# Kernel tuning notes

Measured on AMD Instinct MI355X. Metric: run time of the kernel, lower is better.

## Reference

```python
import jax, jax.numpy as jnp
import numpy as np
import math

EMBED_DIM = 512
NUM_HEADS = 8
B, T = 1, 4096

def setup_inputs() -> dict:
    key = jax.random.key(0)
    ks = jax.random.split(key, 12)
    D = EMBED_DIM
    s = 1.0 / math.sqrt(D)
    inp = {
        "x": jax.random.normal(ks[0], (B, T, D), dtype=jnp.float32),
        "ln1_scale": jnp.ones((D,), jnp.float32),
        "ln1_bias": jnp.zeros((D,), jnp.float32),
        "Wq": jax.random.normal(ks[1], (D, D), jnp.float32) * s,
        "bq": jnp.zeros((D,), jnp.float32),
        "Wk": jax.random.normal(ks[2], (D, D), jnp.float32) * s,
        "bk": jnp.zeros((D,), jnp.float32),
        "Wv": jax.random.normal(ks[3], (D, D), jnp.float32) * s,
        "bv": jnp.zeros((D,), jnp.float32),
        "Wo": jax.random.normal(ks[4], (D, D), jnp.float32) * s,
        "bo": jnp.zeros((D,), jnp.float32),
        "ln2_scale": jnp.ones((D,), jnp.float32),
        "ln2_bias": jnp.zeros((D,), jnp.float32),
        "W1": jax.random.normal(ks[5], (D, 4 * D), jnp.float32) * s,
        "b1": jnp.zeros((4 * D,), jnp.float32),
        "W2": jax.random.normal(ks[6], (4 * D, D), jnp.float32) * (1.0 / math.sqrt(4 * D)),
        "b2": jnp.zeros((D,), jnp.float32),
    }
    return inp

def _layernorm(x, scale, bias, eps=1e-6):
    mu = jnp.mean(x, axis=-1, keepdims=True)
    var = jnp.mean(jnp.square(x - mu), axis=-1, keepdims=True)
    return (x - mu) * jax.lax.rsqrt(var + eps) * scale + bias

def reference(x, ln1_scale, ln1_bias, Wq, bq, Wk, bk, Wv, bv, Wo, bo,
              ln2_scale, ln2_bias, W1, b1, W2, b2):
    Bb, Tt, D = x.shape
    H = NUM_HEADS
    hd = D // H
    residual = x
    h = _layernorm(x, ln1_scale, ln1_bias)
    q = (h @ Wq + bq).reshape(Bb, Tt, H, hd).transpose(0, 2, 1, 3)
    k = (h @ Wk + bk).reshape(Bb, Tt, H, hd).transpose(0, 2, 1, 3)
    v = (h @ Wv + bv).reshape(Bb, Tt, H, hd).transpose(0, 2, 1, 3)
    # [B,H,T,T] scores (naive attention as in the original module)
    scores = jnp.einsum('bhqd,bhkd->bhqk', q, k) / math.sqrt(hd)
    probs = jax.nn.softmax(scores, axis=-1)
    out = jnp.einsum('bhqk,bhkd->bhqd', probs, v).transpose(0, 2, 1, 3).reshape(Bb, Tt, D)
    h = out @ Wo + bo  # dropout deterministic -> identity
    x = h + residual
    residual = x
    h = _layernorm(x, ln2_scale, ln2_bias)
    h = jax.nn.gelu(h @ W1 + b1, approximate=True)
    h = h @ W2 + b2
    return h + residual
```

## Files before the change

kernel.cpp:

```cpp
#include <hip/hip_runtime.h>
#include <hip/hip_bf16.h>
#include <stdint.h>

typedef __bf16 bf16;
typedef __bf16 bf16x4 __attribute__((ext_vector_type(4)));
typedef __bf16 bf16x8 __attribute__((ext_vector_type(8)));
typedef float  f32x4  __attribute__((ext_vector_type(4)));
typedef float  f32x16 __attribute__((ext_vector_type(16)));

#define MFMA32(A_, B_, C_) __builtin_amdgcn_mfma_f32_32x32x16_bf16((A_), (B_), (C_), 0, 0, 0)

#define QSCALE 0.1803368801111137f

__device__ __forceinline__ void gload_lds16(const void* g, void* l) {
  __builtin_amdgcn_global_load_lds(
      (const __attribute__((address_space(1))) unsigned int*)g,
      (__attribute__((address_space(3))) unsigned int*)l, 16, 0, 0);
}

__device__ __forceinline__ unsigned pk2(float lo, float hi_) {
  union { bf16 h[2]; unsigned u; } t;
  t.h[0] = (bf16)lo; t.h[1] = (bf16)hi_;
  return t.u;
}

__device__ __forceinline__ float fast_exp2(float x) {
#if __has_builtin(__builtin_amdgcn_exp2f)
  return __builtin_amdgcn_exp2f(x);
#else
  return exp2f(x);
#endif
}

__global__ __launch_bounds__(256) void prep_ln(const float* __restrict__ Wq,
                                               const float* __restrict__ Wk,
                                               const float* __restrict__ Wv,
                                               const float* __restrict__ Wo,
                                               const float* __restrict__ W1,
                                               const float* __restrict__ W2,
                                               const float* __restrict__ bq,
                                               const float* __restrict__ bk,
                                               const float* __restrict__ bv,
                                               bf16* __restrict__ wqkvT, bf16* __restrict__ woT,
                                               bf16* __restrict__ w1T, bf16* __restrict__ w2T,
                                               float* __restrict__ bqkv,
                                               const float* __restrict__ x,
                                               const float* __restrict__ ln1s,
                                               const float* __restrict__ ln1b,
                                               bf16* __restrict__ h) {
  const int b = blockIdx.x;
  if (b >= 774) {
    const int w = threadIdx.x >> 6, l = threadIdx.x & 63;
    const int row = (b - 774) * 4 + w;
    const float4* xp = (const float4*)(x + (size_t)row * 512 + l * 8);
    float4 v0 = xp[0], v1 = xp[1];
    float xv[8] = {v0.x, v0.y, v0.z, v0.w, v1.x, v1.y, v1.z, v1.w};
    float s = 0.f, q = 0.f;
#pragma unroll
    for (int j = 0; j < 8; ++j) { s += xv[j]; q += xv[j] * xv[j]; }
#pragma unroll
    for (int m = 1; m < 64; m <<= 1) { s += __shfl_xor(s, m); q += __shfl_xor(q, m); }
    const float mean = s * (1.f / 512.f);
    const float var = q * (1.f / 512.f) - mean * mean;
    const float rstd = rsqrtf(var + 1e-6f);
    const float4* scp = (const float4*)(ln1s + l * 8);
    const float4* bip = (const float4*)(ln1b + l * 8);
    float4 s0 = scp[0], s1 = scp[1], b0 = bip[0], b1 = bip[1];
    float sv[8] = {s0.x, s0.y, s0.z, s0.w, s1.x, s1.y, s1.z, s1.w};
    float bvv[8] = {b0.x, b0.y, b0.z, b0.w, b1.x, b1.y, b1.z, b1.w};
    bf16x8 ov;
#pragma unroll
    for (int j = 0; j < 8; ++j) ov[j] = (bf16)((xv[j] - mean) * rstd * sv[j] + bvv[j]);
    *(bf16x8*)(h + (size_t)row * 512 + l * 8) = ov;
    return;
  }
  if (b >= 768) {
    int i = (b - 768) * 256 + threadIdx.x;
    if (i < 1536)
      bqkv[i] = (i < 512) ? bq[i] * QSCALE : (i < 1024 ? bk[i - 512] : bv[i - 1024]);
    return;
  }
  const float* in; bf16* outp; int K, N, t; float sc = 1.f;
  if (b < 64)       { in = Wq; outp = wqkvT;              K = 512;  N = 512;  t = b;       sc = QSCALE; }
  else if (b < 128) { in = Wk; outp = wqkvT + 512 * 512;  K = 512;  N = 512;  t = b - 64;  }
  else if (b < 192) { in = Wv; outp = wqkvT + 1024 * 512; K = 512;  N = 512;  t = b - 128; }
  else if (b < 256) { in = Wo; outp = woT;                K = 512;  N = 512;  t = b - 192; }
  else if (b < 512) { in = W1; outp = w1T;                K = 512;  N = 2048; t = b - 256; }
  else              { in = W2; outp = w2T;                K = 2048; N = 512;  t = b - 512; }
  const int tx = K >> 6;
  const int k0 = (t % tx) * 64, n0 = (t / tx) * 64;
  __shared__ bf16 tile[64][72];
  const int tid = threadIdx.x;
#pragma unroll
  for (int s = 0; s < 16; ++s) {
    int j = tid + s * 256;
    int r = j >> 6, c = j & 63;
    tile[r][c] = (bf16)(in[(size_t)(k0 + r) * N + n0 + c] * sc);
  }
  __syncthreads();
#pragma unroll
  for (int s = 0; s < 16; ++s) {
    int j = tid + s * 256;
    int n = j >> 6, k = j & 63;
    outp[(size_t)(n0 + n) * K + k0 + k] = tile[k][n];
  }
}

__global__ __launch_bounds__(256) void ln_k(const float* __restrict__ x,
                                            const float* __restrict__ sc,
                                            const float* __restrict__ bi,
                                            bf16* __restrict__ out) {
  const int w = threadIdx.x >> 6, l = threadIdx.x & 63;
  const int row = blockIdx.x * 4 + w;
  const float4* xp = (const float4*)(x + (size_t)row * 512 + l * 8);
  float4 v0 = xp[0], v1 = xp[1];
  float xv[8] = {v0.x, v0.y, v0.z, v0.w, v1.x, v1.y, v1.z, v1.w};
  float s = 0.f, q = 0.f;
#pragma unroll
  for (int j = 0; j < 8; ++j) { s += xv[j]; q += xv[j] * xv[j]; }
#pragma unroll
  for (int m = 1; m < 64; m <<= 1) { s += __shfl_xor(s, m); q += __shfl_xor(q, m); }
  const float mean = s * (1.f / 512.f);
  const float var = q * (1.f / 512.f) - mean * mean;
  const float rstd = rsqrtf(var + 1e-6f);
  const float4* scp = (const float4*)(sc + l * 8);
  const float4* bip = (const float4*)(bi + l * 8);
  float4 s0 = scp[0], s1 = scp[1], b0 = bip[0], b1 = bip[1];
  float sv[8] = {s0.x, s0.y, s0.z, s0.w, s1.x, s1.y, s1.z, s1.w};
  float bvv[8] = {b0.x, b0.y, b0.z, b0.w, b1.x, b1.y, b1.z, b1.w};
  bf16x8 ov;
#pragma unroll
  for (int j = 0; j < 8; ++j) ov[j] = (bf16)((xv[j] - mean) * rstd * sv[j] + bvv[j]);
  *(bf16x8*)(out + (size_t)row * 512 + l * 8) = ov;
}

template <int EPI>
__global__ __launch_bounds__(256, 3) void gemm32(const bf16* __restrict__ A,
                                                 const bf16* __restrict__ Bt,
                                                 const float* __restrict__ bias,
                                                 const float* __restrict__ res,
                                                 void* __restrict__ outp,
                                                 bf16* __restrict__ k2,
                                                 bf16* __restrict__ v2,
                                                 int M, int N, int K) {
  __shared__ bf16 a_lds[3][64 * 64];
  __shared__ bf16 b_lds[3][64 * 64];
  const int m0 = blockIdx.x * 64, n0 = blockIdx.y * 64;
  const int tid = threadIdx.x, l = tid & 63, w = tid >> 6;
  const int wm = w >> 1, wn = w & 1;
  const int hi = l >> 5, l5 = l & 31;
  const int lr = l >> 3;
  const int cs = (l & 7) ^ (lr & 7);
  const int swl = l5 & 7;

  const bf16* ag = A + (size_t)(m0 + w * 16 + lr) * K + cs * 8;
  const bf16* bg = Bt + (size_t)(n0 + w * 16 + lr) * K + cs * 8;
  const size_t r8 = (size_t)8 * K;

#define GS32(B_)                                                   \
  do {                                                             \
    gload_lds16(ag,      (char*)a_lds[(B_)] + (w * 16) * 128);     \
    gload_lds16(ag + r8, (char*)a_lds[(B_)] + (w * 16 + 8) * 128); \
    gload_lds16(bg,      (char*)b_lds[(B_)] + (w * 16) * 128);     \
    gload_lds16(bg + r8, (char*)b_lds[(B_)] + (w * 16 + 8) * 128); \
    ag += 64; bg += 64;                                            \
  } while (0)

  f32x16 acc = {};
  const int kiters = K >> 6;
  GS32(0);
  GS32(1);
  asm volatile("s_waitcnt vmcnt(4)" ::: "memory");
  __builtin_amdgcn_s_barrier();
  for (int kt = 0; kt < kiters; ++kt) {
    if (kt + 2 < kiters) GS32((kt + 2) % 3);
    const bf16* ab = a_lds[kt % 3] + (wm * 32 + l5) * 64;
    const bf16* bb = b_lds[kt % 3] + (wn * 32 + l5) * 64;
#pragma unroll
    for (int kk = 0; kk < 4; ++kk) {
      bf16x8 af = *(const bf16x8*)(ab + ((kk * 2 + hi) ^ swl) * 8);
      bf16x8 bf_ = *(const bf16x8*)(bb + ((kk * 2 + hi) ^ swl) * 8);
      acc = MFMA32(bf_, af, acc);
    }
    if (kt + 1 < kiters) {
      if (kt + 2 < kiters) asm volatile("s_waitcnt vmcnt(4)" ::: "memory");
      else                 asm volatile("s_waitcnt vmcnt(0)" ::: "memory");
      __builtin_amdgcn_s_barrier();
    }
  }
#undef GS32

  const int row = m0 + wm * 32 + l5;
  if constexpr (EPI == 1 || EPI == 2) {
#pragma unroll
    for (int rg = 0; rg < 4; ++rg) {
      const int cb = n0 + wn * 32 + rg * 8 + hi * 4;
      float4 bb4 = *(const float4*)(bias + cb);
      float v[4];
      v[0] = acc[rg * 4 + 0] + bb4.x;
      v[1] = acc[rg * 4 + 1] + bb4.y;
      v[2] = acc[rg * 4 + 2] + bb4.z;
      v[3] = acc[rg * 4 + 3] + bb4.w;
      if constexpr (EPI == 1) {
        float4 rr = *(const float4*)(res + (size_t)row * N + cb);
        *(float4*)((float*)outp + (size_t)row * N + cb) =
            make_float4(v[0] + rr.x, v[1] + rr.y, v[2] + rr.z, v[3] + rr.w);
      } else {
        bf16x4 o;
#pragma unroll
        for (int e = 0; e < 4; ++e) {
          float t = -2.3022077697f * (v[e] + 0.044715f * v[e] * v[e] * v[e]);
          o[e] = (bf16)(v[e] / (1.f + fast_exp2(t)));
        }
        *(bf16x4*)((bf16*)outp + (size_t)row * N + cb) = o;
      }
    }
  } else {
    __syncthreads();
    bf16(*ct)[72] = (bf16(*)[72])a_lds;
    const int rl = wm * 32 + l5;
#pragma unroll
    for (int rg = 0; rg < 4; ++rg) {
      const int cl = wn * 32 + rg * 8 + hi * 4;
      float4 bb4 = *(const float4*)(bias + n0 + cl);
      bf16x4 o;
      o[0] = (bf16)(acc[rg * 4 + 0] + bb4.x);
      o[1] = (bf16)(acc[rg * 4 + 1] + bb4.y);
      o[2] = (bf16)(acc[rg * 4 + 2] + bb4.z);
      o[3] = (bf16)(acc[rg * 4 + 3] + bb4.w);
      *(bf16x4*)(&ct[rl][cl]) = o;
    }
    __syncthreads();
    if (n0 < 512) {
#pragma unroll
      for (int p = 0; p < 2; ++p) {
        int idx = p * 256 + tid;
        int r = idx >> 3, c = (idx & 7) * 8;
        *(bf16x8*)((bf16*)outp + (size_t)(m0 + r) * 512 + n0 + c) =
            *(const bf16x8*)(&ct[r][c]);
      }
    } else if (n0 < 1024) {
      bf16* kb = k2 + (size_t)((n0 - 512) >> 6) * 262144 + (size_t)m0 * 64;
#pragma unroll
      for (int p = 0; p < 2; ++p) {
        int idx = p * 256 + tid;
        int r = idx >> 3, c = (idx & 7) * 8;
        *(bf16x8*)(kb + r * 64 + c) = *(const bf16x8*)(&ct[r][c]);
      }
    } else {
      bf16* vb = v2 + (size_t)((n0 - 1024) >> 6) * 262144 + (size_t)(m0 >> 5) * 2048;
      const int d = tid >> 2, t8 = (tid & 3) * 8;
#pragma unroll
      for (int p = 0; p < 2; ++p) {
        bf16x8 vv;
#pragma unroll
        for (int e = 0; e < 8; ++e) vv[e] = ct[p * 32 + t8 + e][d];
        *(bf16x8*)(vb + p * 2048 + d * 32 + t8) = vv;
      }
    }
  }
}

__global__ __launch_bounds__(512, 4) void attn_k(const bf16* __restrict__ q2,
                                                 const bf16* __restrict__ k2,
                                                 const bf16* __restrict__ v2,
                                                 bf16* __restrict__ attnb) {
  const int bid = blockIdx.x;
  const int head = bid & 7;
  const int qt = bid >> 3;
  const int w = threadIdx.x >> 6, l = threadIdx.x & 63;
  const int hi = l >> 5, l5 = l & 31;
  const int pair = w >> 1, wq = w & 1;

  __shared__ __align__(16) char smem[65536];
  char* kt_l = smem + pair * 16384;
  char* vt_l = kt_l + 8192;

  const int qrow0 = qt * 64 + wq * 32;
  const bf16* qb = q2 + (size_t)(qrow0 + l5) * 512 + head * 64;
  bf16x8 qf[4];
#pragma unroll
  for (int cc = 0; cc < 4; ++cc) qf[cc] = *(const bf16x8*)(qb + cc * 16 + hi * 8);

  const int kstart = pair * 1024;

  const int lr = l >> 3;
  const int lc3 = (l & 7) ^ lr;
  const char* kg = (const char*)k2 + (size_t)head * 524288 + (size_t)kstart * 128 +
                   (wq * 16 + lr) * 128 + lc3 * 16;
  const char* vg = (const char*)v2 + (size_t)head * 524288 + (size_t)(kstart >> 5) * 4096 +
                   (lc3 >> 2) * 2048 + (wq * 16 + lr) * 64 + (lc3 & 3) * 16;
  const int kdst = wq * 2048;

#define STAGE(B_)                                                            \
  do {                                                                       \
    gload_lds16(kg,        kt_l + (B_) * 4096 + kdst);                       \
    gload_lds16(kg + 1024, kt_l + (B_) * 4096 + kdst + 1024);                \
    gload_lds16(vg,        vt_l + (B_) * 4096 + kdst);                       \
    gload_lds16(vg + 512,  vt_l + (B_) * 4096 + kdst + 1024);                \
    kg += 4096; vg += 4096;                                                  \
  } while (0)

  STAGE(0);
  __syncthreads();

  f32x16 o0 = {}, o1 = {};
  float psum = 0.f;
  const int swl = l5 & 7;
  const char* kbase = kt_l + l5 * 128;
  const char* vbase = vt_l + l5 * 128;

  for (int t = 0; t < 32; ++t) {
    const int cur = t & 1;
    if (t < 31) STAGE(cur ^ 1);

    __builtin_amdgcn_s_setprio(1);
    f32x16 s = {};
#pragma unroll
    for (int cc = 0; cc < 4; ++cc) {
      bf16x8 kf = *(const bf16x8*)(kbase + cur * 4096 + ((cc * 2 + hi) ^ swl) * 16);
      s = MFMA32(kf, qf[cc], s);
    }
    __builtin_amdgcn_s_setprio(0);

#pragma unroll
    for (int c = 0; c < 2; ++c) {
      float p[8];
#pragma unroll
      for (int j = 0; j < 8; ++j) p[j] = fast_exp2(s[c * 8 + j]);
      psum += ((p[0] + p[1]) + (p[2] + p[3])) + ((p[4] + p[5]) + (p[6] + p[7]));
      unsigned X = pk2(p[0], p[1]), X2 = pk2(p[2], p[3]);
      unsigned Y = pk2(p[4], p[5]), Y2 = pk2(p[6], p[7]);
      asm volatile("v_permlane32_swap_b32 %0, %1" : "+v"(X), "+v"(Y));
      asm volatile("v_permlane32_swap_b32 %0, %1" : "+v"(X2), "+v"(Y2));
      union { unsigned wd[4]; bf16x8 v; } pa;
      pa.wd[0] = X; pa.wd[1] = X2; pa.wd[2] = Y; pa.wd[3] = Y2;
      bf16x8 vf0 = *(const bf16x8*)(vbase + cur * 4096 + ((c * 2 + hi) ^ swl) * 16);
      bf16x8 vf1 = *(const bf16x8*)(vbase + cur * 4096 + ((4 + c * 2 + hi) ^ swl) * 16);
      __builtin_amdgcn_s_setprio(1);
      o0 = MFMA32(vf0, pa.v, o0);
      o1 = MFMA32(vf1, pa.v, o1);
      __builtin_amdgcn_s_setprio(0);
    }
    __syncthreads();
  }
#undef STAGE

  float* comb = (float*)smem;
  if (pair > 0) {
    float* cb = comb + (((pair - 1) * 2 + wq) * 64 + l) * 33;
#pragma unroll
    for (int r = 0; r < 16; ++r) { cb[r] = o0[r]; cb[16 + r] = o1[r]; }
    cb[32] = psum;
  }
  __syncthreads();
  if (pair == 0) {
#pragma unroll
    for (int p = 0; p < 3; ++p) {
      const float* cb = comb + ((p * 2 + wq) * 64 + l) * 33;
#pragma unroll
      for (int r = 0; r < 16; ++r) { o0[r] += cb[r]; o1[r] += cb[16 + r]; }
      psum += cb[32];
    }
    const float lsum = psum + __shfl_xor(psum, 32);
    const float inv = 1.f / lsum;
    bf16* ob = attnb + (size_t)(qrow0 + l5) * 512 + head * 64;
#pragma unroll
    for (int dt = 0; dt < 2; ++dt)
#pragma unroll
      for (int rg = 0; rg < 4; ++rg) {
        bf16x4 vv;
#pragma unroll
        for (int e = 0; e < 4; ++e) {
          const float ov = (dt == 0) ? o0[rg * 4 + e] : o1[rg * 4 + e];
          vv[e] = (bf16)(ov * inv);
        }
        *(bf16x4*)(ob + dt * 32 + rg * 8 + hi * 4) = vv;
      }
  }
}

extern "C" void kernel_launch(void* const* d_in, const int* in_sizes, int n_in,
                              void* d_out, int out_size, void* d_ws, size_t ws_size,
                              hipStream_t stream) {
  const float* x    = (const float*)d_in[0];
  const float* ln1s = (const float*)d_in[1];
  const float* ln1b = (const float*)d_in[2];
  const float* Wq   = (const float*)d_in[3];
  const float* bq   = (const float*)d_in[4];
  const float* Wk   = (const float*)d_in[5];
  const float* bk   = (const float*)d_in[6];
  const float* Wv   = (const float*)d_in[7];
  const float* bv   = (const float*)d_in[8];
  const float* Wo   = (const float*)d_in[9];
  const float* bo   = (const float*)d_in[10];
  const float* ln2s = (const float*)d_in[11];
  const float* ln2b = (const float*)d_in[12];
  const float* W1   = (const float*)d_in[13];
  const float* b1   = (const float*)d_in[14];
  const float* W2   = (const float*)d_in[15];
  const float* b2   = (const float*)d_in[16];
  float* out = (float*)d_out;

  char* ws = (char*)d_ws;
  bf16*  wqkvT = (bf16*)(ws + 0);
  bf16*  woT   = (bf16*)(ws + 1572864);
  bf16*  w1T   = (bf16*)(ws + 2097152);
  bf16*  w2T   = (bf16*)(ws + 4194304);
  float* bqkv  = (float*)(ws + 6291456);
  float* x2    = (float*)(ws + 6297600);
  bf16*  h     = (bf16*)(ws + 14686208);
  bf16*  q2    = (bf16*)(ws + 18880512);
  bf16*  k2    = (bf16*)(ws + 23074816);
  bf16*  v2    = (bf16*)(ws + 27269120);
  bf16*  attnb = h;
  bf16*  h2    = h;
  bf16*  gbuf  = (bf16*)(ws + 18880512);

  prep_ln<<<1798, 256, 0, stream>>>(Wq, Wk, Wv, Wo, W1, W2, bq, bk, bv,
                                    wqkvT, woT, w1T, w2T, bqkv, x, ln1s, ln1b, h);
  gemm32<3><<<dim3(64, 24), 256, 0, stream>>>(h, wqkvT, bqkv, nullptr, q2, k2, v2,
                                              4096, 1536, 512);
  attn_k<<<512, 512, 0, stream>>>(q2, k2, v2, attnb);
  gemm32<1><<<dim3(64, 8), 256, 0, stream>>>(attnb, woT, bo, x, x2, nullptr, nullptr,
                                             4096, 512, 512);
  ln_k<<<1024, 256, 0, stream>>>(x2, ln2s, ln2b, h2);
  gemm32<2><<<dim3(64, 32), 256, 0, stream>>>(h2, w1T, b1, nullptr, gbuf, nullptr, nullptr,
                                              4096, 2048, 512);
  gemm32<1><<<dim3(64, 8), 256, 0, stream>>>(gbuf, w2T, b2, x2, out, nullptr, nullptr,
                                             4096, 512, 2048);
}
```

Before: 140.2 us.

## Add 128x128-tile GEMM kernel for QKV and FFN-up projections

Adds a new GEMM kernel with 128x128 output tiles, where each wave computes a 2x2 grid of 32x32 MFMA tiles, and uses it for the QKV projection and the W1+GELU GEMM. The small 64x64 kernel is kept only for the residual-epilogue GEMMs. The aim is more operand reuse per LDS load and fewer total blocks and global loads for the wider-N GEMMs. The cost is more accumulator registers and fewer blocks: the QKV launch drops to 384 blocks, which may underfill the GPU. The K and V scatter epilogues are rewritten so one tile covers two heads.

Result: faster. 133.0 us (-5.1%).

```diff
diff --git a/kernel.cpp b/kernel.cpp
--- a/kernel.cpp
+++ b/kernel.cpp
@@ -140,8 +140,6 @@
                                                  const float* __restrict__ bias,
                                                  const float* __restrict__ res,
                                                  void* __restrict__ outp,
-                                                 bf16* __restrict__ k2,
-                                                 bf16* __restrict__ v2,
                                                  int M, int N, int K) {
   __shared__ bf16 a_lds[3][64 * 64];
   __shared__ bf16 b_lds[3][64 * 64];
@@ -191,71 +189,161 @@
 #undef GS32
 
   const int row = m0 + wm * 32 + l5;
-  if constexpr (EPI == 1 || EPI == 2) {
-#pragma unroll
-    for (int rg = 0; rg < 4; ++rg) {
-      const int cb = n0 + wn * 32 + rg * 8 + hi * 4;
-      float4 bb4 = *(const float4*)(bias + cb);
-      float v[4];
-      v[0] = acc[rg * 4 + 0] + bb4.x;
-      v[1] = acc[rg * 4 + 1] + bb4.y;
-      v[2] = acc[rg * 4 + 2] + bb4.z;
-      v[3] = acc[rg * 4 + 3] + bb4.w;
-      if constexpr (EPI == 1) {
-        float4 rr = *(const float4*)(res + (size_t)row * N + cb);
-        *(float4*)((float*)outp + (size_t)row * N + cb) =
-            make_float4(v[0] + rr.x, v[1] + rr.y, v[2] + rr.z, v[3] + rr.w);
-      } else {
-        bf16x4 o;
-#pragma unroll
-        for (int e = 0; e < 4; ++e) {
-          float t = -2.3022077697f * (v[e] + 0.044715f * v[e] * v[e] * v[e]);
-          o[e] = (bf16)(v[e] / (1.f + fast_exp2(t)));
+#pragma unroll
+  for (int rg = 0; rg < 4; ++rg) {
+    const int cb = n0 + wn * 32 + rg * 8 + hi * 4;
+    float4 bb4 = *(const float4*)(bias + cb);
+    float v[4];
+    v[0] = acc[rg * 4 + 0] + bb4.x;
+    v[1] = acc[rg * 4 + 1] + bb4.y;
+    v[2] = acc[rg * 4 + 2] + bb4.z;
+    v[3] = acc[rg * 4 + 3] + bb4.w;
+    float4 rr = *(const float4*)(res + (size_t)row * N + cb);
+    *(float4*)((float*)outp + (size_t)row * N + cb) =
+        make_float4(v[0] + rr.x, v[1] + rr.y, v[2] + rr.z, v[3] + rr.w);
+  }
+}
+
+template <int EPI>
+__global__ __launch_bounds__(256, 3) void gemm_w(const bf16* __restrict__ A,
+                                                 const bf16* __restrict__ Bt,
+                                                 const float* __restrict__ bias,
+                                                 void* __restrict__ outp,
+                                                 bf16* __restrict__ k2,
+                                                 bf16* __restrict__ v2,
+                                                 int M, int N, int K) {
+  __shared__ __align__(16) char smem[49152];
+  char* a_lds = smem;
+  char* b_lds = smem + 24576;
+  const int tid = threadIdx.x, l = tid & 63, w = tid >> 6;
+  const int wm = w >> 1, wn = w & 1;
+  const int hi = l >> 5, l5 = l & 31;
+  const int m0 = blockIdx.x * 128, n0 = blockIdx.y * 128;
+  const int swl = l5 & 7;
+
+  const int sr = tid >> 3, sp = tid & 7;
+  const int slc = sp ^ (sr & 7);
+  const int shalf = slc >> 2, skc = slc & 3;
+  const bf16* ag = A + (size_t)(m0 + shalf * 64 + sr) * K + skc * 8;
+  const bf16* bg = Bt + (size_t)(n0 + shalf * 64 + sr) * K + skc * 8;
+  const size_t r32 = (size_t)32 * K;
+
+#define GSW(B_)                                                       \
+  do {                                                                \
+    gload_lds16(ag,       a_lds + (B_) * 8192 + w * 1024);            \
+    gload_lds16(ag + r32, a_lds + (B_) * 8192 + 4096 + w * 1024);     \
+    gload_lds16(bg,       b_lds + (B_) * 8192 + w * 1024);            \
+    gload_lds16(bg + r32, b_lds + (B_) * 8192 + 4096 + w * 1024);     \
+    ag += 32; bg += 32;                                               \
+  } while (0)
+
+  f32x16 acc00 = {}, acc01 = {}, acc10 = {}, acc11 = {};
+  const int kiters = K >> 5;
+  GSW(0);
+  GSW(1);
+  asm volatile("s_waitcnt vmcnt(4)" ::: "memory");
+  __builtin_amdgcn_s_barrier();
+  for (int kt = 0; kt < kiters; ++kt) {
+    if (kt + 2 < kiters) GSW((kt + 2) % 3);
+    const char* ab = a_lds + (kt % 3) * 8192;
+    const char* bb = b_lds + (kt % 3) * 8192;
+#pragma unroll
+    for (int kk = 0; kk < 2; ++kk) {
+      bf16x8 af0 = *(const bf16x8*)(ab + (l5)*128      + ((wm * 4 + kk * 2 + hi) ^ swl) * 16);
+      bf16x8 af1 = *(const bf16x8*)(ab + (32 + l5)*128 + ((wm * 4 + kk * 2 + hi) ^ swl) * 16);
+      bf16x8 bf0 = *(const bf16x8*)(bb + (l5)*128      + ((wn * 4 + kk * 2 + hi) ^ swl) * 16);
+      bf16x8 bf1 = *(const bf16x8*)(bb + (32 + l5)*128 + ((wn * 4 + kk * 2 + hi) ^ swl) * 16);
+      acc00 = MFMA32(bf0, af0, acc00);
+      acc01 = MFMA32(bf1, af0, acc01);
+      acc10 = MFMA32(bf0, af1, acc10);
+      acc11 = MFMA32(bf1, af1, acc11);
+    }
+    if (kt + 1 < kiters) {
+      if (kt + 2 < kiters) asm volatile("s_waitcnt vmcnt(4)" ::: "memory");
+      else                 asm volatile("s_waitcnt vmcnt(0)" ::: "memory");
+      __builtin_amdgcn_s_barrier();
+    }
+  }
+#undef GSW
+
+  if constexpr (EPI == 2) {
+#pragma unroll
+    for (int mi = 0; mi < 2; ++mi) {
+      const int row = m0 + wm * 64 + mi * 32 + l5;
+#pragma unroll
+      for (int ni = 0; ni < 2; ++ni) {
+        const f32x16& ac = (mi == 0) ? (ni == 0 ? acc00 : acc01)
+                                     : (ni == 0 ? acc10 : acc11);
+#pragma unroll
+        for (int rg = 0; rg < 4; ++rg) {
+          const int cb = n0 + wn * 64 + ni * 32 + rg * 8 + hi * 4;
+          float4 bb4 = *(const float4*)(bias + cb);
+          float v[4] = {ac[rg * 4 + 0] + bb4.x, ac[rg * 4 + 1] + bb4.y,
+                        ac[rg * 4 + 2] + bb4.z, ac[rg * 4 + 3] + bb4.w};
+          bf16x4 o;
+#pragma unroll
+          for (int e = 0; e < 4; ++e) {
+            float t = -2.3022077697f * (v[e] + 0.044715f * v[e] * v[e] * v[e]);
+            o[e] = (bf16)(v[e] / (1.f + fast_exp2(t)));
+          }
+          *(bf16x4*)((bf16*)outp + (size_t)row * N + cb) = o;
         }
-        *(bf16x4*)((bf16*)outp + (size_t)row * N + cb) = o;
       }
     }
   } else {
     __syncthreads();
-    bf16(*ct)[72] = (bf16(*)[72])a_lds;
-    const int rl = wm * 32 + l5;
-#pragma unroll
-    for (int rg = 0; rg < 4; ++rg) {
-      const int cl = wn * 32 + rg * 8 + hi * 4;
-      float4 bb4 = *(const float4*)(bias + n0 + cl);
-      bf16x4 o;
-      o[0] = (bf16)(acc[rg * 4 + 0] + bb4.x);
-      o[1] = (bf16)(acc[rg * 4 + 1] + bb4.y);
-      o[2] = (bf16)(acc[rg * 4 + 2] + bb4.z);
-      o[3] = (bf16)(acc[rg * 4 + 3] + bb4.w);
-      *(bf16x4*)(&ct[rl][cl]) = o;
+    bf16(*ct)[136] = (bf16(*)[136])smem;
+#pragma unroll
+    for (int mi = 0; mi < 2; ++mi) {
+      const int rl = wm * 64 + mi * 32 + l5;
+#pragma unroll
+      for (int ni = 0; ni < 2; ++ni) {
+        const f32x16& ac = (mi == 0) ? (ni == 0 ? acc00 : acc01)
+                                     : (ni == 0 ? acc10 : acc11);
+#pragma unroll
+        for (int rg = 0; rg < 4; ++rg) {
+          const int cl = wn * 64 + ni * 32 + rg * 8 + hi * 4;
+          float4 bb4 = *(const float4*)(bias + n0 + cl);
+          bf16x4 o;
+          o[0] = (bf16)(ac[rg * 4 + 0] + bb4.x);
+          o[1] = (bf16)(ac[rg * 4 + 1] + bb4.y);
+          o[2] = (bf16)(ac[rg * 4 + 2] + bb4.z);
+          o[3] = (bf16)(ac[rg * 4 + 3] + bb4.w);
+          *(bf16x4*)(&ct[rl][cl]) = o;
+        }
+      }
     }
     __syncthreads();
     if (n0 < 512) {
 #pragma unroll
-      for (int p = 0; p < 2; ++p) {
-        int idx = p * 256 + tid;
-        int r = idx >> 3, c = (idx & 7) * 8;
-        *(bf16x8*)((bf16*)outp + (size_t)(m0 + r) * 512 + n0 + c) =
-            *(const bf16x8*)(&ct[r][c]);
+      for (int p = 0; p < 8; ++p) {
+        int v = p * 256 + tid;
+        int r = v >> 4, c8 = (v & 15) * 8;
+        *(bf16x8*)((bf16*)outp + (size_t)(m0 + r) * 512 + n0 + c8) =
+            *(const bf16x8*)(&ct[r][c8]);
       }
     } else if (n0 < 1024) {
-      bf16* kb = k2 + (size_t)((n0 - 512) >> 6) * 262144 + (size_t)m0 * 64;
-#pragma unroll
-      for (int p = 0; p < 2; ++p) {
-        int idx = p * 256 + tid;
-        int r = idx >> 3, c = (idx & 7) * 8;
-        *(bf16x8*)(kb + r * 64 + c) = *(const bf16x8*)(&ct[r][c]);
+      const int hb = (n0 - 512) >> 6;
+#pragma unroll
+      for (int p = 0; p < 8; ++p) {
+        int v = p * 256 + tid;
+        int r = v >> 4, c8 = (v & 15) * 8;
+        *(bf16x8*)(k2 + (size_t)(hb + (c8 >> 6)) * 262144 +
+                   (size_t)(m0 + r) * 64 + (c8 & 63)) = *(const bf16x8*)(&ct[r][c8]);
       }
     } else {
-      bf16* vb = v2 + (size_t)((n0 - 1024) >> 6) * 262144 + (size_t)(m0 >> 5) * 2048;
+      const int hb = (n0 - 1024) >> 6;
       const int d = tid >> 2, t8 = (tid & 3) * 8;
 #pragma unroll
-      for (int p = 0; p < 2; ++p) {
-        bf16x8 vv;
-#pragma unroll
-        for (int e = 0; e < 8; ++e) vv[e] = ct[p * 32 + t8 + e][d];
-        *(bf16x8*)(vb + p * 2048 + d * 32 + t8) = vv;
+      for (int h2 = 0; h2 < 2; ++h2) {
+        bf16* vb = v2 + (size_t)(hb + h2) * 262144 + (size_t)(m0 >> 5) * 2048;
+#pragma unroll
+        for (int p = 0; p < 4; ++p) {
+          bf16x8 vv;
+#pragma unroll
+          for (int e = 0; e < 8; ++e) vv[e] = ct[p * 32 + t8 + e][h2 * 64 + d];
+          *(bf16x8*)(vb + p * 2048 + d * 32 + t8) = vv;
+        }
       }
     }
   }
@@ -419,14 +507,12 @@
 
   prep_ln<<<1798, 256, 0, stream>>>(Wq, Wk, Wv, Wo, W1, W2, bq, bk, bv,
                                     wqkvT, woT, w1T, w2T, bqkv, x, ln1s, ln1b, h);
-  gemm32<3><<<dim3(64, 24), 256, 0, stream>>>(h, wqkvT, bqkv, nullptr, q2, k2, v2,
+  gemm_w<3><<<dim3(32, 12), 256, 0, stream>>>(h, wqkvT, bqkv, q2, k2, v2,
                                               4096, 1536, 512);
   attn_k<<<512, 512, 0, stream>>>(q2, k2, v2, attnb);
-  gemm32<1><<<dim3(64, 8), 256, 0, stream>>>(attnb, woT, bo, x, x2, nullptr, nullptr,
-                                             4096, 512, 512);
+  gemm32<1><<<dim3(64, 8), 256, 0, stream>>>(attnb, woT, bo, x, x2, 4096, 512, 512);
   ln_k<<<1024, 256, 0, stream>>>(x2, ln2s, ln2b, h2);
-  gemm32<2><<<dim3(64, 32), 256, 0, stream>>>(h2, w1T, b1, nullptr, gbuf, nullptr, nullptr,
+  gemm_w<2><<<dim3(32, 16), 256, 0, stream>>>(h2, w1T, b1, gbuf, nullptr, nullptr,
                                               4096, 2048, 512);
-  gemm32<1><<<dim3(64, 8), 256, 0, stream>>>(gbuf, w2T, b2, x2, out, nullptr, nullptr,
-                                             4096, 512, 2048);
-}
+  gemm32<1><<<dim3(64, 8), 256, 0, stream>>>(gbuf, w2T, b2, x2, out, 4096, 512, 2048);
+}
```
